# Kernel optimization log

Hardware: AMD Instinct MI355X
Metric: run time of the kernel (lower is better)

The kernel has to match this reference:

```python
import jax, jax.numpy as jnp
import numpy as np

B, S, D, H, F = 2, 2048, 1024, 16, 4096
HD = D // H
EPS = 1e-5


def _layernorm(x, g, b):
    mu = jnp.mean(x, axis=-1, keepdims=True)
    var = jnp.var(x, axis=-1, keepdims=True)
    return (x - mu) * jax.lax.rsqrt(var + EPS) * g + b


def setup_inputs() -> dict:
    key = jax.random.key(0)
    ks = jax.random.split(key, 10)
    sd = 0.02
    return {
        "src": jax.random.normal(ks[0], (B, S, D), jnp.float32),
        "qkv_w": jax.random.normal(ks[1], (3 * D, D), jnp.float32) * sd,
        "qkv_b": jnp.zeros((3 * D,), jnp.float32),
        "out_w": jax.random.normal(ks[2], (D, D), jnp.float32) * sd,
        "out_b": jnp.zeros((D,), jnp.float32),
        "ffn_w1": jax.random.normal(ks[3], (F, D), jnp.float32) * sd,
        "ffn_b1": jnp.zeros((F,), jnp.float32),
        "ffn_w2": jax.random.normal(ks[4], (D, F), jnp.float32) * sd,
        "ffn_b2": jnp.zeros((D,), jnp.float32),
        "ln1_g": jnp.ones((D,), jnp.float32),
        "ln1_b": jnp.zeros((D,), jnp.float32),
        "ln2_g": jnp.ones((D,), jnp.float32),
        "ln2_b": jnp.zeros((D,), jnp.float32),
    }


def reference(src, qkv_w, qkv_b, out_w, out_b, ffn_w1, ffn_b1, ffn_w2, ffn_b2,
              ln1_g, ln1_b, ln2_g, ln2_b):
    # --- Multi-head self-attention (post-norm, dropout=identity in eval) ---
    qkv = src @ qkv_w.T + qkv_b                        # [B,S,3D]
    qkv = qkv.reshape(B, S, H, 3 * HD).transpose(0, 2, 1, 3)  # [B,H,S,3hd]
    q, k, v = jnp.split(qkv, 3, axis=-1)               # each [B,H,S,hd]
    scores = jnp.einsum('bhqd,bhkd->bhqk', q, k) / np.sqrt(HD).astype(np.float32)
    attn = jax.nn.softmax(scores, axis=-1)
    ctx = jnp.einsum('bhqk,bhkd->bhqd', attn, v)       # [B,H,S,hd]
    ctx = ctx.transpose(0, 2, 1, 3).reshape(B, S, D)
    mha_out = ctx @ out_w.T + out_b
    agg = _layernorm(src + mha_out, ln1_g, ln1_b)
    # --- FFN: Linear -> ReLU -> Linear ---
    h = jax.nn.relu(agg @ ffn_w1.T + ffn_b1)
    ffn_out = h @ ffn_w2.T + ffn_b2
    return _layernorm(agg + ffn_out, ln2_g, ln2_b)
```

## Files before the change

### kernel.cpp

```cpp
#include <hip/hip_runtime.h>


typedef unsigned short u16;
typedef unsigned int u32;
typedef __attribute__((ext_vector_type(8))) __bf16 bf16x8;
typedef __attribute__((ext_vector_type(4))) float f32x4;
typedef __attribute__((ext_vector_type(4))) short s16x4;
typedef __attribute__((ext_vector_type(2))) u32 u32x2;

__device__ __forceinline__ u16 f2bf(float f) {
  u32 u = __float_as_uint(f);
  u += 0x7fffu + ((u >> 16) & 1u);
  return (u16)(u >> 16);
}

__device__ __forceinline__ u32 pk_bf_trunc(float a, float b) {
  return (__float_as_uint(a) >> 16) | (__float_as_uint(b) & 0xffff0000u);
}

__device__ __forceinline__ void async16(const void* g, void* l) {
  __builtin_amdgcn_global_load_lds((__attribute__((address_space(1))) void*)g,
                                   (__attribute__((address_space(3))) void*)l,
                                   16, 0, 0);
}

__device__ __forceinline__ f32x4 mfma16(bf16x8 a, bf16x8 b, f32x4 c) {
  return __builtin_amdgcn_mfma_f32_16x16x32_bf16(a, b, c, 0, 0, 0);
}

__device__ __forceinline__ f32x4 mfma_pv(s16x4 a, s16x4 b, f32x4 c) {
#if __has_builtin(__builtin_amdgcn_mfma_f32_16x16x16bf16_1k)
  return __builtin_amdgcn_mfma_f32_16x16x16bf16_1k(a, b, c, 0, 0, 0);
#else
  f32x4 d;
  asm("v_mfma_f32_16x16x16_bf16 %0, %1, %2, %3" : "=v"(d) : "v"(a), "v"(b), "v"(c));
  return d;
#endif
}

__global__ __launch_bounds__(256) void cvt_bf16(const float* __restrict__ in,
                                                u16* __restrict__ out) {
  int i = blockIdx.x * 256 + threadIdx.x;
  float4 v = ((const float4*)in)[i];
  ushort4 o;
  o.x = f2bf(v.x); o.y = f2bf(v.y); o.z = f2bf(v.z); o.w = f2bf(v.w);
  ((ushort4*)out)[i] = o;
}

template <int MODE, int SPLIT>
__global__ __launch_bounds__(256)
void gemm_bt(const u16* __restrict__ A, const u16* __restrict__ W,
             const float* __restrict__ bias,
             float* __restrict__ outf, u16* __restrict__ outb,
             u16* __restrict__ qo, u16* __restrict__ ko, u16* __restrict__ vto,
             int M, int N, int K) {
  __shared__ u16 As[128 * 32];
  __shared__ u16 Bs[128 * 32];
  const int lane = threadIdx.x & 63;
  const int wave = threadIdx.x >> 6;
  const int lrow = lane & 15;
  const int lq = lane >> 4;
  const int tm = blockIdx.x * 128;
  const int tn = blockIdx.y * 128;
  const int wm = (wave >> 1) * 64;
  const int wn = (wave & 1) * 64;
  const int kc = K / SPLIT;
  const int kbeg = blockIdx.z * kc;
  f32x4 acc[4][4] = {};

  for (int k0 = kbeg; k0 < kbeg + kc; k0 += 32) {
#pragma unroll
    for (int c = 0; c < 2; ++c) {
      int chunk = wave * 128 + c * 64 + lane;
      int row = chunk >> 2;
      int sc = chunk & 3;
      int cc = sc ^ ((row >> 1) & 3);
      u16* la = As + (size_t)(wave * 128 + c * 64) * 8;
      u16* lb = Bs + (size_t)(wave * 128 + c * 64) * 8;
      async16(A + (size_t)(tm + row) * K + (k0 + cc * 8), la);
      async16(W + (size_t)(tn + row) * K + (k0 + cc * 8), lb);
    }
    __syncthreads();
    bf16x8 a_frag[4], b_frag[4];
#pragma unroll
    for (int i = 0; i < 4; ++i) {
      int row = wm + i * 16 + lrow;
      int sc = lq ^ ((row >> 1) & 3);
      a_frag[i] = *(const bf16x8*)(As + row * 32 + sc * 8);
    }
#pragma unroll
    for (int j = 0; j < 4; ++j) {
      int row = wn + j * 16 + lrow;
      int sc = lq ^ ((row >> 1) & 3);
      b_frag[j] = *(const bf16x8*)(Bs + row * 32 + sc * 8);
    }
#pragma unroll
    for (int i = 0; i < 4; ++i)
#pragma unroll
      for (int j = 0; j < 4; ++j)
        acc[i][j] = mfma16(a_frag[i], b_frag[j], acc[i][j]);
    __syncthreads();
  }

  float* outp = outf;
  if constexpr (MODE == 0) {
    if constexpr (SPLIT > 1) outp += (size_t)blockIdx.z * M * N;
  }

#pragma unroll
  for (int i = 0; i < 4; ++i) {
#pragma unroll
    for (int j = 0; j < 4; ++j) {
      int col = tn + wn + j * 16 + lrow;
      float bv = (SPLIT == 1 || blockIdx.z == 0) ? bias[col] : 0.f;
#pragma unroll
      for (int r = 0; r < 4; ++r) {
        int row = tm + wm + i * 16 + lq * 4 + r;
        float v = acc[i][j][r] + bv;
        if constexpr (MODE == 0) {
          outp[(size_t)row * N + col] = v;
        } else if constexpr (MODE == 1) {
          outb[(size_t)row * N + col] = f2bf(fmaxf(v, 0.f));
        } else {
          int b = row >> 11, s = row & 2047;
          int h = col / 192, c = col - h * 192;
          size_t tok = (size_t)(b * 16 + h) * 2048 + s;
          if (c < 64)
            qo[tok * 64 + c] = f2bf(v * 0.1803368801f);
          else if (c < 128)
            ko[tok * 64 + (c - 64)] = f2bf(v);
          else
            vto[((size_t)(b * 16 + h) * 64 + (c - 128)) * 2048 + s] = f2bf(v);
        }
      }
    }
  }
}

__global__ __launch_bounds__(512)
void attn_kernel(const u16* __restrict__ Q, const u16* __restrict__ K,
                 const u16* __restrict__ Vt, u16* __restrict__ ctx) {
  __shared__ u16 Ks[128 * 64];
  __shared__ u16 Vs[64 * 128];
  const int tid = threadIdx.x;
  const int lane = tid & 63;
  const int wave = tid >> 6;
  const int wq = wave & 3;
  const int half = wave >> 2;
  const int lrow = lane & 15;
  const int q = lane >> 4;
  const int qb = blockIdx.x;
  const int bh = blockIdx.y;
  const u16* Qp = Q + ((size_t)bh * 2048 + qb * 128 + half * 64) * 64;
  const u16* Kp = K + (size_t)bh * 2048 * 64;
  const u16* Vp = Vt + (size_t)bh * 64 * 2048;

  bf16x8 qf[2];
#pragma unroll
  for (int kk = 0; kk < 2; ++kk)
    qf[kk] = *(const bf16x8*)(Qp + (wq * 16 + lrow) * 64 + kk * 32 + q * 8);

  f32x4 oacc[4] = {};
  float l_i = 0.f;

  for (int kb = 0; kb < 16; ++kb) {
    if (half == 0) {
#pragma unroll
      for (int t = 0; t < 4; ++t) {
        int c = wq * 256 + t * 64 + lane;
        int row = c >> 3, sc = c & 7;
        int cc = sc ^ (row & 7);
        async16(Kp + (size_t)(kb * 128 + row) * 64 + cc * 8,
                Ks + (size_t)(wq * 256 + t * 64) * 8);
      }
    } else {
#pragma unroll
      for (int t = 0; t < 4; ++t) {
        int c = wq * 256 + t * 64 + lane;
        int row = c >> 4, sc = c & 15;
        int cc = sc ^ (row & 7);
        async16(Vp + (size_t)row * 2048 + kb * 128 + cc * 8,
                Vs + (size_t)(wq * 256 + t * 64) * 8);
      }
    }
    __syncthreads();

    f32x4 sacc[8] = {};
#pragma unroll
    for (int j = 0; j < 8; ++j) {
#pragma unroll
      for (int kk = 0; kk < 2; ++kk) {
        int row = j * 16 + lrow;
        int sc = (kk * 4 + q) ^ (row & 7);
        bf16x8 kf = *(const bf16x8*)(Ks + row * 64 + sc * 8);
        sacc[j] = mfma16(kf, qf[kk], sacc[j]);
      }
    }

    float ps = 0.f;
#pragma unroll
    for (int j = 0; j < 8; ++j)
#pragma unroll
      for (int r = 0; r < 4; ++r) {
        float p = exp2f(sacc[j][r]);
        sacc[j][r] = p;
        ps += p;
      }
    ps += __shfl_xor(ps, 16);
    ps += __shfl_xor(ps, 32);
    l_i += ps;

    s16x4 pa[8];
#pragma unroll
    for (int j = 0; j < 8; ++j) {
      u32x2 pw;
      pw.x = pk_bf_trunc(sacc[j][0], sacc[j][1]);
      pw.y = pk_bf_trunc(sacc[j][2], sacc[j][3]);
      pa[j] = __builtin_bit_cast(s16x4, pw);
    }

#pragma unroll
    for (int j = 0; j < 8; ++j) {
#pragma unroll
      for (int jn = 0; jn < 4; ++jn) {
        int row = jn * 16 + lrow;
        int sc = (j * 2 + (q >> 1)) ^ (row & 7);
        s16x4 vb = *(const s16x4*)(Vs + row * 128 + sc * 8 + (q & 1) * 4);
        oacc[jn] = mfma_pv(pa[j], vb, oacc[jn]);
      }
    }
    __syncthreads();
  }

  float linv = 1.f / l_i;
  const int b = bh >> 4, h = bh & 15;
#pragma unroll
  for (int r = 0; r < 4; ++r) {
    float lr = __shfl(linv, q * 4 + r);
    int s = qb * 128 + half * 64 + wq * 16 + q * 4 + r;
    size_t base = ((size_t)(b * 2048 + s)) * 1024 + h * 64;
#pragma unroll
    for (int jn = 0; jn < 4; ++jn)
      ctx[base + jn * 16 + lrow] = f2bf(oacc[jn][r] * lr);
  }
}

template <int P>
__global__ __launch_bounds__(256)
void ln_kernel(const float* __restrict__ x1, const float* __restrict__ x2,
               const float* __restrict__ g, const float* __restrict__ bb,
               float* __restrict__ outf, u16* __restrict__ outb) {
  const int t = blockIdx.x;
  const int tid = threadIdx.x;
  const int lane = tid & 63, wave = tid >> 6;
  const size_t base = (size_t)t * 1024;
  const size_t pstride = 4096ull * 1024;
  float v[4];
  float s = 0.f, s2 = 0.f;
#pragma unroll
  for (int e = 0; e < 4; ++e) {
    int i = tid + e * 256;
    float x = x1[base + i];
#pragma unroll
    for (int p = 0; p < P; ++p) x += x2[p * pstride + base + i];
    v[e] = x;
    s += x;
    s2 += x * x;
  }
#pragma unroll
  for (int d = 1; d < 64; d <<= 1) {
    s += __shfl_xor(s, d);
    s2 += __shfl_xor(s2, d);
  }
  __shared__ float red[8];
  if (lane == 0) { red[wave] = s; red[4 + wave] = s2; }
  __syncthreads();
  s = red[0] + red[1] + red[2] + red[3];
  s2 = red[4] + red[5] + red[6] + red[7];
  float mean = s * (1.f / 1024.f);
  float var = s2 * (1.f / 1024.f) - mean * mean;
  float rstd = rsqrtf(var + 1e-5f);
#pragma unroll
  for (int e = 0; e < 4; ++e) {
    int i = tid + e * 256;
    float y = (v[e] - mean) * rstd * g[i] + bb[i];
    outf[base + i] = y;
    if (outb) outb[base + i] = f2bf(y);
  }
}

extern "C" void kernel_launch(void* const* d_in, const int* in_sizes, int n_in,
                              void* d_out, int out_size, void* d_ws, size_t ws_size,
                              hipStream_t stream) {
  const float* src    = (const float*)d_in[0];
  const float* qkv_w  = (const float*)d_in[1];
  const float* qkv_b  = (const float*)d_in[2];
  const float* out_w  = (const float*)d_in[3];
  const float* out_b  = (const float*)d_in[4];
  const float* ffn_w1 = (const float*)d_in[5];
  const float* ffn_b1 = (const float*)d_in[6];
  const float* ffn_w2 = (const float*)d_in[7];
  const float* ffn_b2 = (const float*)d_in[8];
  const float* ln1_g  = (const float*)d_in[9];
  const float* ln1_b  = (const float*)d_in[10];
  const float* ln2_g  = (const float*)d_in[11];
  const float* ln2_b  = (const float*)d_in[12];

  char* ws = (char*)d_ws;
  size_t off = 0;
  auto alloc = [&](size_t bytes) -> void* {
    void* p = ws + off;
    off += (bytes + 255) & ~(size_t)255;
    return p;
  };
  u16* wqkv = (u16*)alloc(3072ull * 1024 * 2);
  u16* wout = (u16*)alloc(1024ull * 1024 * 2);
  u16* wf1  = (u16*)alloc(4096ull * 1024 * 2);
  u16* wf2  = (u16*)alloc(1024ull * 4096 * 2);
  u16* srcb = (u16*)alloc(4096ull * 1024 * 2);
  u16* qb_  = (u16*)alloc(32ull * 2048 * 64 * 2);
  u16* kb_  = (u16*)alloc(32ull * 2048 * 64 * 2);
  u16* vtb  = (u16*)alloc(32ull * 64 * 2048 * 2);
  u16* ctxb = (u16*)alloc(4096ull * 1024 * 2);
  float* mha  = (float*)alloc(4ull * 4096 * 1024 * 4);
  float* aggf = (float*)alloc(4096ull * 1024 * 4);
  u16* aggb = (u16*)alloc(4096ull * 1024 * 2);
  u16* hb   = (u16*)alloc(4096ull * 4096 * 2);
  float* ffnf = (float*)alloc(4ull * 4096 * 1024 * 4);

  cvt_bf16<<<3072 * 1024 / 1024, 256, 0, stream>>>(qkv_w, wqkv);
  cvt_bf16<<<1024 * 1024 / 1024, 256, 0, stream>>>(out_w, wout);
  cvt_bf16<<<4096 * 1024 / 1024, 256, 0, stream>>>(ffn_w1, wf1);
  cvt_bf16<<<4096 * 1024 / 1024, 256, 0, stream>>>(ffn_w2, wf2);
  cvt_bf16<<<4096 * 1024 / 1024, 256, 0, stream>>>(src, srcb);

  gemm_bt<2, 1><<<dim3(32, 24), 256, 0, stream>>>(srcb, wqkv, qkv_b, nullptr, nullptr,
                                                  qb_, kb_, vtb, 4096, 3072, 1024);
  attn_kernel<<<dim3(16, 32), 512, 0, stream>>>(qb_, kb_, vtb, ctxb);
  gemm_bt<0, 4><<<dim3(32, 8, 4), 256, 0, stream>>>(ctxb, wout, out_b, mha, nullptr,
                                                    nullptr, nullptr, nullptr, 4096, 1024, 1024);
  ln_kernel<4><<<4096, 256, 0, stream>>>(src, mha, ln1_g, ln1_b, aggf, aggb);
  gemm_bt<1, 1><<<dim3(32, 32), 256, 0, stream>>>(aggb, wf1, ffn_b1, nullptr, hb,
                                                  nullptr, nullptr, nullptr, 4096, 4096, 1024);
  gemm_bt<0, 4><<<dim3(32, 8, 4), 256, 0, stream>>>(hb, wf2, ffn_b2, ffnf, nullptr,
                                                    nullptr, nullptr, nullptr, 4096, 1024, 4096);
  ln_kernel<4><<<4096, 256, 0, stream>>>(aggf, ffnf, ln2_g, ln2_b, (float*)d_out, nullptr);
}
```

Baseline: 423.8 us.

## Double GEMM K-step to 64 and store split-K partials as bf16

Each GEMM iteration now stages a 64-wide K slice in shared memory, using an 8-way XOR swizzle, and runs two MFMA sub-steps per barrier pair. This halves the number of sync and load rounds per tile. Split-K partial outputs for the out-projection and FFN2 are now written as bf16 instead of fp32, and the layernorm kernel reads them back as bf16. This halves partial-buffer traffic, but each partial is rounded to bf16 before it is summed, which adds some precision loss.

```diff
diff --git a/kernel.cpp b/kernel.cpp
--- a/kernel.cpp
+++ b/kernel.cpp
@@ -12,6 +12,10 @@
   u32 u = __float_as_uint(f);
   u += 0x7fffu + ((u >> 16) & 1u);
   return (u16)(u >> 16);
+}
+
+__device__ __forceinline__ float bf2f(u16 h) {
+  return __uint_as_float((u32)h << 16);
 }
 
 __device__ __forceinline__ u32 pk_bf_trunc(float a, float b) {
@@ -51,11 +55,11 @@
 __global__ __launch_bounds__(256)
 void gemm_bt(const u16* __restrict__ A, const u16* __restrict__ W,
              const float* __restrict__ bias,
-             float* __restrict__ outf, u16* __restrict__ outb,
+             u16* __restrict__ outb,
              u16* __restrict__ qo, u16* __restrict__ ko, u16* __restrict__ vto,
              int M, int N, int K) {
-  __shared__ u16 As[128 * 32];
-  __shared__ u16 Bs[128 * 32];
+  __shared__ u16 As[128 * 64];
+  __shared__ u16 Bs[128 * 64];
   const int lane = threadIdx.x & 63;
   const int wave = threadIdx.x >> 6;
   const int lrow = lane & 15;
@@ -68,44 +72,45 @@
   const int kbeg = blockIdx.z * kc;
   f32x4 acc[4][4] = {};
 
-  for (int k0 = kbeg; k0 < kbeg + kc; k0 += 32) {
-#pragma unroll
-    for (int c = 0; c < 2; ++c) {
-      int chunk = wave * 128 + c * 64 + lane;
-      int row = chunk >> 2;
-      int sc = chunk & 3;
-      int cc = sc ^ ((row >> 1) & 3);
-      u16* la = As + (size_t)(wave * 128 + c * 64) * 8;
-      u16* lb = Bs + (size_t)(wave * 128 + c * 64) * 8;
+  for (int k0 = kbeg; k0 < kbeg + kc; k0 += 64) {
+#pragma unroll
+    for (int c = 0; c < 4; ++c) {
+      int chunk = wave * 256 + c * 64 + lane;
+      int row = chunk >> 3;
+      int sc = chunk & 7;
+      int cc = sc ^ (row & 7);
+      u16* la = As + (size_t)(wave * 256 + c * 64) * 8;
+      u16* lb = Bs + (size_t)(wave * 256 + c * 64) * 8;
       async16(A + (size_t)(tm + row) * K + (k0 + cc * 8), la);
       async16(W + (size_t)(tn + row) * K + (k0 + cc * 8), lb);
     }
     __syncthreads();
-    bf16x8 a_frag[4], b_frag[4];
-#pragma unroll
-    for (int i = 0; i < 4; ++i) {
-      int row = wm + i * 16 + lrow;
-      int sc = lq ^ ((row >> 1) & 3);
-      a_frag[i] = *(const bf16x8*)(As + row * 32 + sc * 8);
-    }
-#pragma unroll
-    for (int j = 0; j < 4; ++j) {
-      int row = wn + j * 16 + lrow;
-      int sc = lq ^ ((row >> 1) & 3);
-      b_frag[j] = *(const bf16x8*)(Bs + row * 32 + sc * 8);
-    }
-#pragma unroll
-    for (int i = 0; i < 4; ++i)
-#pragma unroll
-      for (int j = 0; j < 4; ++j)
-        acc[i][j] = mfma16(a_frag[i], b_frag[j], acc[i][j]);
+#pragma unroll
+    for (int h = 0; h < 2; ++h) {
+      bf16x8 a_frag[4], b_frag[4];
+#pragma unroll
+      for (int i = 0; i < 4; ++i) {
+        int row = wm + i * 16 + lrow;
+        int sc = (h * 4 + lq) ^ (row & 7);
+        a_frag[i] = *(const bf16x8*)(As + row * 64 + sc * 8);
+      }
+#pragma unroll
+      for (int j = 0; j < 4; ++j) {
+        int row = wn + j * 16 + lrow;
+        int sc = (h * 4 + lq) ^ (row & 7);
+        b_frag[j] = *(const bf16x8*)(Bs + row * 64 + sc * 8);
+      }
+#pragma unroll
+      for (int i = 0; i < 4; ++i)
+#pragma unroll
+        for (int j = 0; j < 4; ++j)
+          acc[i][j] = mfma16(a_frag[i], b_frag[j], acc[i][j]);
+    }
     __syncthreads();
   }
 
-  float* outp = outf;
-  if constexpr (MODE == 0) {
-    if constexpr (SPLIT > 1) outp += (size_t)blockIdx.z * M * N;
-  }
+  u16* outp = outb;
+  if constexpr (MODE == 0) outp += (size_t)blockIdx.z * M * N;
 
 #pragma unroll
   for (int i = 0; i < 4; ++i) {
@@ -118,9 +123,9 @@
         int row = tm + wm + i * 16 + lq * 4 + r;
         float v = acc[i][j][r] + bv;
         if constexpr (MODE == 0) {
-          outp[(size_t)row * N + col] = v;
+          outp[(size_t)row * N + col] = f2bf(v);
         } else if constexpr (MODE == 1) {
-          outb[(size_t)row * N + col] = f2bf(fmaxf(v, 0.f));
+          outp[(size_t)row * N + col] = f2bf(fmaxf(v, 0.f));
         } else {
           int b = row >> 11, s = row & 2047;
           int h = col / 192, c = col - h * 192;
@@ -247,7 +252,7 @@
 
 template <int P>
 __global__ __launch_bounds__(256)
-void ln_kernel(const float* __restrict__ x1, const float* __restrict__ x2,
+void ln_kernel(const float* __restrict__ x1, const u16* __restrict__ x2,
                const float* __restrict__ g, const float* __restrict__ bb,
                float* __restrict__ outf, u16* __restrict__ outb) {
   const int t = blockIdx.x;
@@ -262,7 +267,7 @@
     int i = tid + e * 256;
     float x = x1[base + i];
 #pragma unroll
-    for (int p = 0; p < P; ++p) x += x2[p * pstride + base + i];
+    for (int p = 0; p < P; ++p) x += bf2f(x2[p * pstride + base + i]);
     v[e] = x;
     s += x;
     s2 += x * x;
@@ -322,11 +327,11 @@
   u16* kb_  = (u16*)alloc(32ull * 2048 * 64 * 2);
   u16* vtb  = (u16*)alloc(32ull * 64 * 2048 * 2);
   u16* ctxb = (u16*)alloc(4096ull * 1024 * 2);
-  float* mha  = (float*)alloc(4ull * 4096 * 1024 * 4);
+  u16* mha  = (u16*)alloc(4ull * 4096 * 1024 * 2);
   float* aggf = (float*)alloc(4096ull * 1024 * 4);
   u16* aggb = (u16*)alloc(4096ull * 1024 * 2);
   u16* hb   = (u16*)alloc(4096ull * 4096 * 2);
-  float* ffnf = (float*)alloc(4ull * 4096 * 1024 * 4);
+  u16* ffnf = (u16*)alloc(4ull * 4096 * 1024 * 2);
 
   cvt_bf16<<<3072 * 1024 / 1024, 256, 0, stream>>>(qkv_w, wqkv);
   cvt_bf16<<<1024 * 1024 / 1024, 256, 0, stream>>>(out_w, wout);
@@ -334,15 +339,15 @@
   cvt_bf16<<<4096 * 1024 / 1024, 256, 0, stream>>>(ffn_w2, wf2);
   cvt_bf16<<<4096 * 1024 / 1024, 256, 0, stream>>>(src, srcb);
 
-  gemm_bt<2, 1><<<dim3(32, 24), 256, 0, stream>>>(srcb, wqkv, qkv_b, nullptr, nullptr,
+  gemm_bt<2, 1><<<dim3(32, 24), 256, 0, stream>>>(srcb, wqkv, qkv_b, nullptr,
                                                   qb_, kb_, vtb, 4096, 3072, 1024);
   attn_kernel<<<dim3(16, 32), 512, 0, stream>>>(qb_, kb_, vtb, ctxb);
-  gemm_bt<0, 4><<<dim3(32, 8, 4), 256, 0, stream>>>(ctxb, wout, out_b, mha, nullptr,
+  gemm_bt<0, 4><<<dim3(32, 8, 4), 256, 0, stream>>>(ctxb, wout, out_b, mha,
                                                     nullptr, nullptr, nullptr, 4096, 1024, 1024);
   ln_kernel<4><<<4096, 256, 0, stream>>>(src, mha, ln1_g, ln1_b, aggf, aggb);
-  gemm_bt<1, 1><<<dim3(32, 32), 256, 0, stream>>>(aggb, wf1, ffn_b1, nullptr, hb,
+  gemm_bt<1, 1><<<dim3(32, 32), 256, 0, stream>>>(aggb, wf1, ffn_b1, hb,
                                                   nullptr, nullptr, nullptr, 4096, 4096, 1024);
-  gemm_bt<0, 4><<<dim3(32, 8, 4), 256, 0, stream>>>(hb, wf2, ffn_b2, ffnf, nullptr,
+  gemm_bt<0, 4><<<dim3(32, 8, 4), 256, 0, stream>>>(hb, wf2, ffn_b2, ffnf,
                                                     nullptr, nullptr, nullptr, 4096, 1024, 4096);
   ln_kernel<4><<<4096, 256, 0, stream>>>(aggf, ffnf, ln2_g, ln2_b, (float*)d_out, nullptr);
 }
```

Result: faster. 399.8 us (-5.7%).
